# Performance work log

Hardware: AMD Instinct MI355X
Metric: run time of the kernel (lower is better)

Reference implementation:

```python
import jax, jax.numpy as jnp
import numpy as np

LN_EPS = 1e-3  # keras LayerNormalization default epsilon
LEAKY_SLOPE = 0.2  # tf 'leaky_relu' default alpha


def layer_norm(x, gamma, beta):
    mu = jnp.mean(x, axis=-1, keepdims=True)
    var = jnp.mean(jnp.square(x - mu), axis=-1, keepdims=True)
    return (x - mu) * jax.lax.rsqrt(var + LN_EPS) * gamma + beta


def attention_head(q_in, kv_in, Wk, Wv, Wq, causal):
    # q_in: [b, sq, d], kv_in: [b, sk, d]
    K = jnp.einsum('bsd,de->bse', kv_in, Wk)
    V = jnp.einsum('bsd,de->bse', kv_in, Wv)
    Q = jnp.einsum('bsd,de->bse', q_in, Wq)
    sk = K.shape[1]
    # NOTE: original scales by sqrt(window_size_keys), i.e. key seq length
    scores = jnp.einsum('bqe,bke->bqk', Q, K) / jnp.sqrt(jnp.float32(sk))
    if causal:
        sq = Q.shape[1]
        mask = jnp.triu(jnp.full((sq, sk), -jnp.inf, dtype=scores.dtype), k=1)
        scores = scores + mask
    probs = jax.nn.softmax(scores, axis=-1)
    return jnp.einsum('bqk,bke->bqe', probs, V)


def setup_inputs() -> dict:
    key = jax.random.key(0)
    ks = jax.random.split(key, 12)
    B, S, D, H = 4, 4096, 256, 400
    p = lambda k, shp: jax.random.normal(k, shp, dtype=jnp.float32) * 0.1
    return {
        'inputs': jax.random.normal(ks[0], (B, S, D), dtype=jnp.float32),
        'context_sequence': jax.random.normal(ks[1], (B, S, D), dtype=jnp.float32),
        'sa_Wk': p(ks[2], (D, D)),
        'sa_Wv': p(ks[3], (D, D)),
        'sa_Wq': p(ks[4], (D, D)),
        'ca_Wk': p(ks[5], (D, D)),
        'ca_Wv': p(ks[6], (D, D)),
        'ca_Wq': p(ks[7], (D, D)),
        'W1': p(ks[8], (D, H)),
        'b1': jnp.zeros((H,), dtype=jnp.float32),
        'W2': p(ks[9], (H, D)),
        'b2': jnp.zeros((D,), dtype=jnp.float32),
        'gamma': jnp.ones((D,), dtype=jnp.float32),
        'beta': jnp.zeros((D,), dtype=jnp.float32),
    }


def reference(inputs, context_sequence, sa_Wk, sa_Wv, sa_Wq, ca_Wk, ca_Wv, ca_Wq,
              W1, b1, W2, b2, gamma, beta):
    # 1) masked self-attention + residual + LN (shared LN params)
    in_attn = attention_head(inputs, inputs, sa_Wk, sa_Wv, sa_Wq, causal=True)
    x = layer_norm(in_attn + inputs, gamma, beta)
    # 2) unmasked cross-attention (queries = x, keys/values = context) + residual + LN
    ctx_attn = attention_head(x, context_sequence, ca_Wk, ca_Wv, ca_Wq, causal=False)
    y = layer_norm(ctx_attn + x, gamma, beta)
    # 3) FFN (Dense 400 leaky_relu -> Dense emb) + residual + LN
    h = jax.nn.leaky_relu(jnp.einsum('bsd,dh->bsh', y, W1) + b1, negative_slope=LEAKY_SLOPE)
    ff = jnp.einsum('bsh,hd->bsd', h, W2) + b2
    return layer_norm(ff + y, gamma, beta)
```

## Files before the change

kernel.cpp:

```cpp
#include <hip/hip_runtime.h>

typedef __bf16  bf16x4 __attribute__((ext_vector_type(4)));
typedef __bf16  bf16x8 __attribute__((ext_vector_type(8)));
typedef float   f32x4  __attribute__((ext_vector_type(4)));
typedef unsigned int u32;

constexpr int BM = 128, BN = 128, BK = 32;

__device__ __forceinline__ void async_cp16(const __bf16* g, __bf16* lds) {
    __builtin_amdgcn_global_load_lds(
        (const __attribute__((address_space(1))) u32*)g,
        (__attribute__((address_space(3))) u32*)lds, 16, 0, 0);
}

__device__ __forceinline__ int swz(int row, int q) {
    return row * BK + (((q + (row >> 1)) & 3) << 3);
}

template<int EPI>
__launch_bounds__(256)
__global__ void gemm_nt(const __bf16* __restrict__ Aall, const __bf16* __restrict__ Ball,
                        const float* __restrict__ bias,
                        void* __restrict__ C0, void* __restrict__ C1, void* __restrict__ C2,
                        int N, int K, long ldb, long sA, long sB, long sC,
                        int nTx, int klen, long pstrideB)
{
    const int bx = blockIdx.x;
    const int chunk = bx / nTx;
    const int n0 = (bx - chunk * nTx) * BN;
    const int m0 = blockIdx.y * BM;
    const int bz = blockIdx.z;
    const int kbase = chunk * klen;

    const __bf16* A  = Aall + (long)bz * sA;
    const __bf16* Bt = Ball + (long)bz * sB;

    __shared__ alignas(16) __bf16 As[BM * BK];
    __shared__ alignas(16) __bf16 Bs[BN * BK];

    const int tid = threadIdx.x;
    const int wave = tid >> 6, lane = tid & 63;
    const int wm = (wave >> 1) * 64, wn = (wave & 1) * 64;
    const int quad = lane >> 4, l16 = lane & 15;

    const int row0 = tid >> 2, sl0 = tid & 3;
    const int ks0 = (sl0 - (row0 >> 1)) & 3;
    const int row1 = row0 + 64;
    const int ks1 = (sl0 - (row1 >> 1)) & 3;
    const __bf16* gA0 = A  + (long)(m0 + row0) * K + kbase + ks0 * 8;
    const __bf16* gA1 = A  + (long)(m0 + row1) * K + kbase + ks1 * 8;
    const __bf16* gB0 = Bt + (long)(n0 + row0) * ldb + kbase + ks0 * 8;
    const __bf16* gB1 = Bt + (long)(n0 + row1) * ldb + kbase + ks1 * 8;
    __bf16* ldsA0 = As + wave * 512;
    __bf16* ldsA1 = As + 2048 + wave * 512;
    __bf16* ldsB0 = Bs + wave * 512;
    __bf16* ldsB1 = Bs + 2048 + wave * 512;

    f32x4 acc[4][4];
    #pragma unroll
    for (int i = 0; i < 4; i++)
        #pragma unroll
        for (int j = 0; j < 4; j++) { f32x4 z = {0.f, 0.f, 0.f, 0.f}; acc[i][j] = z; }

    for (int kk = 0; kk < klen; kk += BK) {
        __syncthreads();
        async_cp16(gA0, ldsA0);
        async_cp16(gA1, ldsA1);
        async_cp16(gB0, ldsB0);
        async_cp16(gB1, ldsB1);
        gA0 += BK; gA1 += BK; gB0 += BK; gB1 += BK;
        __syncthreads();

        bf16x8 af[4], bg[4];
        #pragma unroll
        for (int i = 0; i < 4; i++) {
            af[i] = *(const bf16x8*)(As + swz(wm + i * 16 + l16, quad));
            bg[i] = *(const bf16x8*)(Bs + swz(wn + i * 16 + l16, quad));
        }
        #pragma unroll
        for (int i = 0; i < 4; i++)
            #pragma unroll
            for (int j = 0; j < 4; j++)
                acc[i][j] = __builtin_amdgcn_mfma_f32_16x16x32_bf16(af[i], bg[j], acc[i][j], 0, 0, 0);
    }

    char* cb = (char*)C0 + (EPI == 3 ? (long)chunk * pstrideB : 0);
    #pragma unroll
    for (int j = 0; j < 4; j++) {
        const int col = n0 + wn + j * 16 + l16;
        const float bv = (EPI == 2) ? bias[col] : 0.f;
        #pragma unroll
        for (int i = 0; i < 4; i++) {
            #pragma unroll
            for (int r = 0; r < 4; r++) {
                const int row = m0 + wm + i * 16 + quad * 4 + r;
                float c = acc[i][j][r];
                if (EPI == 2) { c += bv; c = c > 0.f ? c : 0.2f * c; }
                if (EPI == 1 || EPI == 3)
                    ((__bf16*)cb)[(long)bz * sC + (long)row * N + col] = (__bf16)c;
                else if (EPI == 2)
                    ((__bf16*)cb)[(long)row * N + col] = (__bf16)c;
                else {
                    const int seg = col >> 8;
                    __bf16* dst = seg == 0 ? (__bf16*)C0 : (seg == 1 ? (__bf16*)C1 : (__bf16*)C2);
                    dst[(long)row * 256 + (col & 255)] = (__bf16)c;
                }
            }
        }
    }
}

template<int CAUSAL>
__launch_bounds__(512, 2)
__global__ void fattn(const __bf16* __restrict__ Qall, const __bf16* __restrict__ Kall,
                      const __bf16* __restrict__ Vt,
                      __bf16* __restrict__ pbuf, float* __restrict__ side,
                      int NS, long pstrideE, float scale)
{
    constexpr int S = 4096, D = 256, R = 16384;
    const int mt = CAUSAL ? (int)(gridDim.x - 1 - blockIdx.x) : (int)blockIdx.x;
    const int chunk = blockIdx.y;
    const int bz = blockIdx.z;
    const int m0 = mt * 128;

    const int T = CAUSAL ? ((m0 + 128) >> 6) : (S >> 6);
    const int t0 = chunk * T / NS;
    const int t1 = (chunk + 1) * T / NS;
    const int kbase = t0 << 6;
    const int ntile = t1 - t0;

    const __bf16* Q  = Qall + ((long)bz * S + m0) * D;
    const __bf16* Kp = Kall + (long)bz * S * D;
    const long vcol0 = (long)bz * S;

    __shared__ alignas(16) __bf16 Ks[2][16384];
    __shared__ alignas(16) __bf16 Vs[2][16384];
    __shared__ alignas(16) __bf16 Ps[128 * 64];
    __shared__ float sred[8][32];

    const int tid = threadIdx.x;
    const int wave = tid >> 6, lane = tid & 63;
    const int quad = lane >> 4, l16 = lane & 15;
    const int wq32 = (wave >> 1) * 32;
    const int wk = (wave & 1) * 32;
    const int we = (wave & 1) * 128;

    bf16x8 qf[2][8];
    #pragma unroll
    for (int i = 0; i < 2; i++)
        #pragma unroll
        for (int kd = 0; kd < 8; kd++)
            qf[i][kd] = *(const bf16x8*)(Q + (long)(wq32 + i * 16 + l16) * D + kd * 32 + quad * 8);

    const int srowK = (tid >> 2) & 63;
    const int srowV = tid >> 2;
    const int ks8 = (((tid & 3) - (tid >> 3)) & 3) << 3;
    const int wbase = (tid & ~63) * 8;

    f32x4 acc[2][8];
    #pragma unroll
    for (int i = 0; i < 2; i++)
        #pragma unroll
        for (int j = 0; j < 8; j++) { f32x4 z = {0.f, 0.f, 0.f, 0.f}; acc[i][j] = z; }
    float se[2][4] = {{0.f,0.f,0.f,0.f},{0.f,0.f,0.f,0.f}};

    auto stage = [&](int buf, int kb) {
        const __bf16* gK = Kp + (long)(kb + srowK) * D + ks8 + ((tid >> 8) << 5);
        #pragma unroll
        for (int c = 0; c < 4; c++)
            async_cp16(gK + c * 64, Ks[buf] + c * 4096 + wbase);
        const __bf16* gV = Vt + vcol0 + kb + ks8;
        #pragma unroll
        for (int c = 0; c < 4; c++)
            async_cp16(gV + (long)(((c & 1) << 7) + srowV) * R + ((c >> 1) << 5),
                       Vs[buf] + c * 4096 + wbase);
    };

    if (ntile > 0) stage(0, kbase);

    for (int t = 0; t < ntile; ++t) {
        __syncthreads();
        const int kb = kbase + (t << 6);
        if (t + 1 < ntile) stage((t + 1) & 1, kb + 64);

        const __bf16* Kb_ = Ks[t & 1];
        const __bf16* Vb_ = Vs[t & 1];

        f32x4 sacc[2][2];
        #pragma unroll
        for (int i = 0; i < 2; i++)
            #pragma unroll
            for (int j = 0; j < 2; j++) { f32x4 z = {0.f, 0.f, 0.f, 0.f}; sacc[i][j] = z; }
        #pragma unroll
        for (int kd = 0; kd < 8; kd++) {
            bf16x8 b0 = *(const bf16x8*)(Kb_ + kd * 2048 + swz(wk + l16, quad));
            bf16x8 b1 = *(const bf16x8*)(Kb_ + kd * 2048 + swz(wk + 16 + l16, quad));
            sacc[0][0] = __builtin_amdgcn_mfma_f32_16x16x32_bf16(qf[0][kd], b0, sacc[0][0], 0, 0, 0);
            sacc[1][0] = __builtin_amdgcn_mfma_f32_16x16x32_bf16(qf[1][kd], b0, sacc[1][0], 0, 0, 0);
            sacc[0][1] = __builtin_amdgcn_mfma_f32_16x16x32_bf16(qf[0][kd], b1, sacc[0][1], 0, 0, 0);
            sacc[1][1] = __builtin_amdgcn_mfma_f32_16x16x32_bf16(qf[1][kd], b1, sacc[1][1], 0, 0, 0);
        }

        const bool diag = CAUSAL && (kb >= m0);
        #pragma unroll
        for (int i = 0; i < 2; i++)
            #pragma unroll
            for (int j = 0; j < 2; j++) {
                const int kloc = wk + j * 16 + l16;
                #pragma unroll
                for (int r = 0; r < 4; r++) {
                    const int qloc = wq32 + i * 16 + quad * 4 + r;
                    float e = __expf(sacc[i][j][r] * scale);
                    if (diag && kb + kloc > m0 + qloc) e = 0.f;
                    se[i][r] += e;
                    Ps[qloc * 64 + (((kloc >> 3) ^ (qloc & 7)) << 3) + (kloc & 7)] = (__bf16)e;
                }
            }
        __syncthreads();

        #pragma unroll
        for (int kc = 0; kc < 2; kc++) {
            const int sx = (kc * 4 + quad) ^ (l16 & 7);
            bf16x8 pa0 = *(const bf16x8*)(Ps + (wq32 + l16) * 64 + (sx << 3));
            bf16x8 pa1 = *(const bf16x8*)(Ps + (wq32 + 16 + l16) * 64 + (sx << 3));
            #pragma unroll
            for (int jn = 0; jn < 8; jn++) {
                bf16x8 vb = *(const bf16x8*)(Vb_ + kc * 8192 + swz(we + jn * 16 + l16, quad));
                acc[0][jn] = __builtin_amdgcn_mfma_f32_16x16x32_bf16(pa0, vb, acc[0][jn], 0, 0, 0);
                acc[1][jn] = __builtin_amdgcn_mfma_f32_16x16x32_bf16(pa1, vb, acc[1][jn], 0, 0, 0);
            }
        }
    }

    #pragma unroll
    for (int st = 1; st < 16; st <<= 1)
        #pragma unroll
        for (int i = 0; i < 2; i++)
            #pragma unroll
            for (int r = 0; r < 4; r++) se[i][r] += __shfl_xor(se[i][r], st);
    if (l16 == 0)
        #pragma unroll
        for (int i = 0; i < 2; i++)
            #pragma unroll
            for (int r = 0; r < 4; r++)
                sred[wave][i * 16 + quad * 4 + r] = se[i][r];
    __syncthreads();
    if ((wave & 1) == 0 && l16 == 0) {
        float* sd = side + ((long)bz * 64 + chunk) * 4096 + m0 + wq32;
        #pragma unroll
        for (int i = 0; i < 2; i++)
            #pragma unroll
            for (int r = 0; r < 4; r++) {
                const int idx = i * 16 + quad * 4 + r;
                sd[idx] = sred[wave][idx] + sred[wave + 1][idx];
            }
    }

    __bf16* cb = pbuf + (long)chunk * pstrideE + ((long)bz * S + m0) * D;
    #pragma unroll
    for (int jn = 0; jn < 8; jn++) {
        const int col = we + jn * 16 + l16;
        #pragma unroll
        for (int i = 0; i < 2; i++)
            #pragma unroll
            for (int r = 0; r < 4; r++)
                cb[(long)(wq32 + i * 16 + quad * 4 + r) * D + col] = (__bf16)acc[i][jn][r];
    }
}

__global__ void reduce_inv_n(const float* __restrict__ side, float* __restrict__ inv, int lim)
{
    const int i = blockIdx.x * 256 + threadIdx.x;
    const int b = i >> 12, r = i & 4095;
    const float* sp = side + (long)b * 64 * 4096 + r;
    float s = 0.f;
    for (int t = 0; t < lim; t++) s += sp[(long)t * 4096];
    inv[i] = 1.f / s;
}

template<int NP>
__launch_bounds__(256)
__global__ void ln_res(const __bf16* __restrict__ p, long pstr,
                       const float* __restrict__ resid, const float* __restrict__ invs,
                       const float* __restrict__ bias,
                       const float* __restrict__ gamma, const float* __restrict__ beta,
                       float* __restrict__ outf, __bf16* __restrict__ outb)
{
    const int row  = blockIdx.x * 4 + (threadIdx.x >> 6);
    const int lane = threadIdx.x & 63;
    const long vi = (long)row * 64 + lane;
    float p0 = 0.f, p1 = 0.f, p2 = 0.f, p3 = 0.f;
    #pragma unroll
    for (int i = 0; i < NP; i++) {
        bf16x4 vp = ((const bf16x4*)(p + (long)i * pstr))[vi];
        p0 += (float)vp[0]; p1 += (float)vp[1]; p2 += (float)vp[2]; p3 += (float)vp[3];
    }
    if (invs) { const float iv = invs[row]; p0 *= iv; p1 *= iv; p2 *= iv; p3 *= iv; }
    float4 vr = ((const float4*)resid)[vi];
    float x0 = vr.x + p0, x1 = vr.y + p1, x2 = vr.z + p2, x3 = vr.w + p3;
    if (bias) {
        float4 vb = ((const float4*)bias)[lane];
        x0 += vb.x; x1 += vb.y; x2 += vb.z; x3 += vb.w;
    }
    float s = x0 + x1 + x2 + x3;
    #pragma unroll
    for (int off = 32; off; off >>= 1) s += __shfl_xor(s, off);
    const float mu = s * (1.f / 256.f);
    float d0 = x0 - mu, d1 = x1 - mu, d2 = x2 - mu, d3 = x3 - mu;
    float s2 = d0 * d0 + d1 * d1 + d2 * d2 + d3 * d3;
    #pragma unroll
    for (int off = 32; off; off >>= 1) s2 += __shfl_xor(s2, off);
    const float rs = rsqrtf(s2 * (1.f / 256.f) + 1e-3f);
    const float4 g  = ((const float4*)gamma)[lane];
    const float4 be = ((const float4*)beta)[lane];
    float o0 = d0 * rs * g.x + be.x, o1 = d1 * rs * g.y + be.y;
    float o2 = d2 * rs * g.z + be.z, o3 = d3 * rs * g.w + be.w;
    float4 o; o.x = o0; o.y = o1; o.z = o2; o.w = o3;
    ((float4*)outf)[vi] = o;
    if (outb) {
        bf16x4 ob; ob[0] = (__bf16)o0; ob[1] = (__bf16)o1; ob[2] = (__bf16)o2; ob[3] = (__bf16)o3;
        ((bf16x4*)outb)[vi] = ob;
    }
}

__device__ __forceinline__ void tp(const float* __restrict__ src, __bf16* __restrict__ dst,
                                   int rows, int cols, int rowsP, int i)
{
    const int c = i / rowsP, r = i - c * rowsP;
    const float v = (r < rows && c < cols) ? src[r * cols + c] : 0.f;
    dst[i] = (__bf16)v;
}

__global__ void prep_all(const float4* __restrict__ inA, const float4* __restrict__ inC,
                         bf16x4* __restrict__ outA, bf16x4* __restrict__ outC,
                         const float* __restrict__ sWq, const float* __restrict__ sWk,
                         const float* __restrict__ sWv,
                         const float* __restrict__ cWq, const float* __restrict__ cWk,
                         const float* __restrict__ cWv,
                         const float* __restrict__ W1, const float* __restrict__ W2,
                         __bf16* __restrict__ wqk_s, __bf16* __restrict__ wv_s,
                         __bf16* __restrict__ wq_c, __bf16* __restrict__ wk_c,
                         __bf16* __restrict__ wv_c,
                         __bf16* __restrict__ W1t, __bf16* __restrict__ W2t,
                         const float* __restrict__ b1, float* __restrict__ b1p)
{
    const int bx = blockIdx.x, tid = threadIdx.x;
    if (bx < 8192) {
        const bool a = bx < 4096;
        const long j = (long)(a ? bx : bx - 4096) * 256 + tid;
        float4 v = (a ? inA : inC)[j];
        bf16x4 o; o[0] = (__bf16)v.x; o[1] = (__bf16)v.y; o[2] = (__bf16)v.z; o[3] = (__bf16)v.w;
        (a ? outA : outC)[j] = o;
    }
    else if (bx < 8448)  tp(sWq, wqk_s,          256, 256, 256, (bx - 8192)  * 256 + tid);
    else if (bx < 8704)  tp(sWk, wqk_s + 65536,  256, 256, 256, (bx - 8448)  * 256 + tid);
    else if (bx < 8960)  tp(sWv, wv_s,           256, 256, 256, (bx - 8704)  * 256 + tid);
    else if (bx < 9216)  tp(cWq, wq_c,           256, 256, 256, (bx - 8960)  * 256 + tid);
    else if (bx < 9472)  tp(cWk, wk_c,           256, 256, 256, (bx - 9216)  * 256 + tid);
    else if (bx < 9728)  tp(cWv, wv_c,           256, 256, 256, (bx - 9472)  * 256 + tid);
    else if (bx < 10240) tp(W1,  W1t,            256, 400, 256, (bx - 9728)  * 256 + tid);
    else if (bx < 10752) tp(W2,  W2t,            400, 256, 512, (bx - 10240) * 256 + tid);
    else { const int i = (bx - 10752) * 256 + tid; if (i < 512) b1p[i] = (i < 400) ? b1[i] : 0.f; }
}

extern "C" void kernel_launch(void* const* d_in, const int* in_sizes, int n_in,
                              void* d_out, int out_size, void* d_ws, size_t ws_size,
                              hipStream_t stream)
{
    constexpr int B = 4, S = 4096, D = 256, H = 400, Hp = 512;
    constexpr int R = B * S;
    constexpr float SCALE = 1.f / 64.f;
    constexpr int NSc = 4;
    constexpr int NSx = 2;
    constexpr int NSf = 2;

    const float* inputs = (const float*)d_in[0];
    const float* ctx    = (const float*)d_in[1];
    const float* sa_Wk  = (const float*)d_in[2];
    const float* sa_Wv  = (const float*)d_in[3];
    const float* sa_Wq  = (const float*)d_in[4];
    const float* ca_Wk  = (const float*)d_in[5];
    const float* ca_Wv  = (const float*)d_in[6];
    const float* ca_Wq  = (const float*)d_in[7];
    const float* W1     = (const float*)d_in[8];
    const float* b1     = (const float*)d_in[9];
    const float* W2     = (const float*)d_in[10];
    const float* b2     = (const float*)d_in[11];
    const float* gamma  = (const float*)d_in[12];
    const float* beta   = (const float*)d_in[13];
    float* out = (float*)d_out;

    char* ws = (char*)d_ws;
    size_t off = 0;
    auto alloc = [&](size_t bytes) -> char* {
        char* p = ws + off; off += (bytes + 255) & ~size_t(255); return p;
    };
    __bf16* bfA  = (__bf16*)alloc((size_t)R * D * 2);
    __bf16* bfC  = (__bf16*)alloc((size_t)R * D * 2);
    __bf16* Qb   = (__bf16*)alloc((size_t)R * D * 2);
    __bf16* Kb   = (__bf16*)alloc((size_t)R * D * 2);
    __bf16* Vt   = (__bf16*)alloc((size_t)D * R * 2);
    __bf16* h    = (__bf16*)alloc((size_t)R * Hp * 2);
    float*  x    = (float*)alloc((size_t)R * D * 4);
    float*  y    = (float*)alloc((size_t)R * D * 4);
    float*  side = (float*)alloc((size_t)B * 64 * S * 4);
    float*  invb = (float*)alloc((size_t)B * S * 4);
    __bf16* wqk_s = (__bf16*)alloc((size_t)2 * D * D * 2);
    __bf16* wv_s  = (__bf16*)alloc((size_t)D * D * 2);
    __bf16* wq_c  = (__bf16*)alloc((size_t)D * D * 2);
    __bf16* wk_c  = (__bf16*)alloc((size_t)D * D * 2);
    __bf16* wv_c  = (__bf16*)alloc((size_t)D * D * 2);
    __bf16* W1t  = (__bf16*)alloc((size_t)Hp * D * 2);
    __bf16* W2t  = (__bf16*)alloc((size_t)D * Hp * 2);
    float*  b1p  = (float*)alloc((size_t)Hp * 4);

    const size_t PBb = (size_t)R * D * 2;
    __bf16* pbuf = (__bf16*)alloc((size_t)4 * PBb);
    if (off > ws_size) return;
    const long PBe = (long)R * D;

    __bf16* xbf = bfA;
    __bf16* ybf = bfC;

    const dim3 blk(256);
    const dim3 blk512(512);

    auto launch_ln = [&](int np, const float* res, const float* invs, const float* bias,
                         float* of, __bf16* ob) {
        if (np == 4)      ln_res<4><<<R / 4, blk, 0, stream>>>(pbuf, PBe, res, invs, bias, gamma, beta, of, ob);
        else if (np == 2) ln_res<2><<<R / 4, blk, 0, stream>>>(pbuf, PBe, res, invs, bias, gamma, beta, of, ob);
        else              ln_res<1><<<R / 4, blk, 0, stream>>>(pbuf, PBe, res, invs, bias, gamma, beta, of, ob);
    };

    prep_all<<<10754, blk, 0, stream>>>((const float4*)inputs, (const float4*)ctx,
        (bf16x4*)bfA, (bf16x4*)bfC, sa_Wq, sa_Wk, sa_Wv, ca_Wq, ca_Wk, ca_Wv, W1, W2,
        wqk_s, wv_s, wq_c, wk_c, wv_c, W1t, W2t, b1, b1p);

    gemm_nt<4><<<dim3(4, 128, 1), blk, 0, stream>>>(bfA, wqk_s, nullptr,
        Qb, Kb, nullptr, 2 * D, D, D, 0, 0, 0, 4, D, 0);
    gemm_nt<1><<<dim3(128, 2, 1), blk, 0, stream>>>(wv_s, bfA, nullptr,
        Vt, nullptr, nullptr, R, D, D, 0, 0, 0, 128, D, 0);
    fattn<1><<<dim3(32, NSc, B), blk512, 0, stream>>>(Qb, Kb, Vt, pbuf, side, NSc, PBe, SCALE);
    reduce_inv_n<<<R / 256, blk, 0, stream>>>(side, invb, NSc);
    launch_ln(NSc, inputs, invb, nullptr, x, xbf);

    gemm_nt<1><<<dim3(2, 128, 1), blk, 0, stream>>>(xbf, wq_c, nullptr,
        Qb, nullptr, nullptr, D, D, D, 0, 0, 0, 2, D, 0);
    gemm_nt<1><<<dim3(2, 128, 1), blk, 0, stream>>>(bfC, wk_c, nullptr,
        Kb, nullptr, nullptr, D, D, D, 0, 0, 0, 2, D, 0);
    gemm_nt<1><<<dim3(128, 2, 1), blk, 0, stream>>>(wv_c, bfC, nullptr,
        Vt, nullptr, nullptr, R, D, D, 0, 0, 0, 128, D, 0);
    fattn<0><<<dim3(32, NSx, B), blk512, 0, stream>>>(Qb, Kb, Vt, pbuf, side, NSx, PBe, SCALE);
    reduce_inv_n<<<R / 256, blk, 0, stream>>>(side, invb, NSx);
    launch_ln(NSx, x, invb, nullptr, y, ybf);

    gemm_nt<2><<<dim3(4, 128, 1), blk, 0, stream>>>(ybf, W1t, b1p,
        h, nullptr, nullptr, Hp, D, D, 0, 0, 0, 4, D, 0);
    gemm_nt<3><<<dim3(2 * NSf, 128, 1), blk, 0, stream>>>(h, W2t, nullptr,
        pbuf, nullptr, nullptr, D, Hp, Hp, 0, 0, 0, 2, Hp / NSf, (long)PBb);
    launch_ln(NSf, y, nullptr, b2, out, nullptr);
}
```

Before: 409.6 us.

## Prefetch two K/V tiles ahead with fine-grained waitcnt barriers in attention loop

Restructures the attention K/V loop so two tiles are in flight. After each tile is consumed, the next-next tile is staged into the freed buffer, and the loop waits only on vmcnt for the older tile instead of a full __syncthreads. It also raises wave priority around the MFMA sections with s_setprio. This aims to hide global-to-LDS latency better, at the cost of extra barriers per iteration and reliance on manual vmcnt counts matching the number of outstanding loads.

```diff
diff --git a/kernel.cpp b/kernel.cpp
--- a/kernel.cpp
+++ b/kernel.cpp
@@ -16,6 +16,11 @@
 __device__ __forceinline__ int swz(int row, int q) {
     return row * BK + (((q + (row >> 1)) & 3) << 3);
 }
+
+#define ASM_LGKM0 asm volatile("s_waitcnt lgkmcnt(0)" ::: "memory")
+#define ASM_VM8   asm volatile("s_waitcnt vmcnt(8)" ::: "memory")
+#define ASM_VM0   asm volatile("s_waitcnt vmcnt(0)" ::: "memory")
+#define SBAR()    do { __builtin_amdgcn_s_barrier(); asm volatile("" ::: "memory"); } while (0)
 
 template<int EPI>
 __launch_bounds__(256)
@@ -176,21 +181,25 @@
                        Vs[buf] + c * 4096 + wbase);
     };
 
-    if (ntile > 0) stage(0, kbase);
+    if (ntile > 0) {
+        stage(0, kbase);
+        if (ntile > 1) { stage(1, kbase + 64); ASM_VM8; }
+        else           { ASM_VM0; }
+        SBAR();
+    }
 
     for (int t = 0; t < ntile; ++t) {
-        __syncthreads();
+        const int cur = t & 1;
         const int kb = kbase + (t << 6);
-        if (t + 1 < ntile) stage((t + 1) & 1, kb + 64);
-
-        const __bf16* Kb_ = Ks[t & 1];
-        const __bf16* Vb_ = Vs[t & 1];
+        const __bf16* Kb_ = Ks[cur];
+        const __bf16* Vb_ = Vs[cur];
 
         f32x4 sacc[2][2];
         #pragma unroll
         for (int i = 0; i < 2; i++)
             #pragma unroll
             for (int j = 0; j < 2; j++) { f32x4 z = {0.f, 0.f, 0.f, 0.f}; sacc[i][j] = z; }
+        __builtin_amdgcn_s_setprio(1);
         #pragma unroll
         for (int kd = 0; kd < 8; kd++) {
             bf16x8 b0 = *(const bf16x8*)(Kb_ + kd * 2048 + swz(wk + l16, quad));
@@ -200,6 +209,7 @@
             sacc[0][1] = __builtin_amdgcn_mfma_f32_16x16x32_bf16(qf[0][kd], b1, sacc[0][1], 0, 0, 0);
             sacc[1][1] = __builtin_amdgcn_mfma_f32_16x16x32_bf16(qf[1][kd], b1, sacc[1][1], 0, 0, 0);
         }
+        __builtin_amdgcn_s_setprio(0);
 
         const bool diag = CAUSAL && (kb >= m0);
         #pragma unroll
@@ -216,8 +226,9 @@
                     Ps[qloc * 64 + (((kloc >> 3) ^ (qloc & 7)) << 3) + (kloc & 7)] = (__bf16)e;
                 }
             }
-        __syncthreads();
-
+        ASM_LGKM0; SBAR();
+
+        __builtin_amdgcn_s_setprio(1);
         #pragma unroll
         for (int kc = 0; kc < 2; kc++) {
             const int sx = (kc * 4 + quad) ^ (l16 & 7);
@@ -229,6 +240,14 @@
                 acc[0][jn] = __builtin_amdgcn_mfma_f32_16x16x32_bf16(pa0, vb, acc[0][jn], 0, 0, 0);
                 acc[1][jn] = __builtin_amdgcn_mfma_f32_16x16x32_bf16(pa1, vb, acc[1][jn], 0, 0, 0);
             }
+        }
+        __builtin_amdgcn_s_setprio(0);
+        ASM_LGKM0; SBAR();
+
+        if (t + 1 < ntile) {
+            if (t + 2 < ntile) { stage(cur, kbase + ((t + 2) << 6)); ASM_VM8; }
+            else               { ASM_VM0; }
+            SBAR();
         }
     }
 
```

Result: no change. 406.8 us (-0.7%).

## Halve attention key tile to 32 to raise occupancy and split cross-attn further

Applied to the files above, without the earlier changes.

Shrinks the flash-attention key/value tile from 64 to 32 keys. This halves the K/V/P shared-memory buffers and the score accumulators, and the launch bounds now request 4 blocks per CU instead of 2. The P buffer swizzle and the staging index math are reworked for the narrower tile. The cross-attention key split count also goes from 2 to 4. In exchange there are twice as many tile iterations, each with two barriers and less MFMA work to hide latency, and more partial results to combine.

```diff
diff --git a/kernel.cpp b/kernel.cpp
--- a/kernel.cpp
+++ b/kernel.cpp
@@ -111,7 +111,7 @@
 }
 
 template<int CAUSAL>
-__launch_bounds__(512, 2)
+__launch_bounds__(512, 4)
 __global__ void fattn(const __bf16* __restrict__ Qall, const __bf16* __restrict__ Kall,
                       const __bf16* __restrict__ Vt,
                       __bf16* __restrict__ pbuf, float* __restrict__ side,
@@ -123,26 +123,26 @@
     const int bz = blockIdx.z;
     const int m0 = mt * 128;
 
-    const int T = CAUSAL ? ((m0 + 128) >> 6) : (S >> 6);
+    const int T = CAUSAL ? ((m0 + 128) >> 5) : (S >> 5);
     const int t0 = chunk * T / NS;
     const int t1 = (chunk + 1) * T / NS;
-    const int kbase = t0 << 6;
+    const int kbase = t0 << 5;
     const int ntile = t1 - t0;
 
     const __bf16* Q  = Qall + ((long)bz * S + m0) * D;
     const __bf16* Kp = Kall + (long)bz * S * D;
     const long vcol0 = (long)bz * S;
 
-    __shared__ alignas(16) __bf16 Ks[2][16384];
-    __shared__ alignas(16) __bf16 Vs[2][16384];
-    __shared__ alignas(16) __bf16 Ps[128 * 64];
+    __shared__ alignas(16) __bf16 Ks[2][8192];
+    __shared__ alignas(16) __bf16 Vs[2][8192];
+    __shared__ alignas(16) __bf16 Ps[128 * 32];
     __shared__ float sred[8][32];
 
     const int tid = threadIdx.x;
     const int wave = tid >> 6, lane = tid & 63;
     const int quad = lane >> 4, l16 = lane & 15;
     const int wq32 = (wave >> 1) * 32;
-    const int wk = (wave & 1) * 32;
+    const int wk16 = (wave & 1) * 16;
     const int we = (wave & 1) * 128;
 
     bf16x8 qf[2][8];
@@ -152,7 +152,7 @@
         for (int kd = 0; kd < 8; kd++)
             qf[i][kd] = *(const bf16x8*)(Q + (long)(wq32 + i * 16 + l16) * D + kd * 32 + quad * 8);
 
-    const int srowK = (tid >> 2) & 63;
+    const int srowK = (tid >> 2) & 31;
     const int srowV = tid >> 2;
     const int ks8 = (((tid & 3) - (tid >> 3)) & 3) << 3;
     const int wbase = (tid & ~63) * 8;
@@ -165,67 +165,57 @@
     float se[2][4] = {{0.f,0.f,0.f,0.f},{0.f,0.f,0.f,0.f}};
 
     auto stage = [&](int buf, int kb) {
-        const __bf16* gK = Kp + (long)(kb + srowK) * D + ks8 + ((tid >> 8) << 5);
-        #pragma unroll
-        for (int c = 0; c < 4; c++)
-            async_cp16(gK + c * 64, Ks[buf] + c * 4096 + wbase);
-        const __bf16* gV = Vt + vcol0 + kb + ks8;
-        #pragma unroll
-        for (int c = 0; c < 4; c++)
-            async_cp16(gV + (long)(((c & 1) << 7) + srowV) * R + ((c >> 1) << 5),
-                       Vs[buf] + c * 4096 + wbase);
+        const __bf16* gK = Kp + (long)(kb + srowK) * D + ks8 + ((tid >> 7) << 5);
+        async_cp16(gK,       Ks[buf] + wbase);
+        async_cp16(gK + 128, Ks[buf] + 4096 + wbase);
+        const __bf16* gV = Vt + vcol0 + kb + ks8 + (long)srowV * R;
+        async_cp16(gV,                 Vs[buf] + wbase);
+        async_cp16(gV + (long)128 * R, Vs[buf] + 4096 + wbase);
     };
 
     if (ntile > 0) stage(0, kbase);
 
     for (int t = 0; t < ntile; ++t) {
+        const int cur = t & 1;
+        const int kb = kbase + (t << 5);
         __syncthreads();
-        const int kb = kbase + (t << 6);
-        if (t + 1 < ntile) stage((t + 1) & 1, kb + 64);
-
-        const __bf16* Kb_ = Ks[t & 1];
-        const __bf16* Vb_ = Vs[t & 1];
-
-        f32x4 sacc[2][2];
-        #pragma unroll
-        for (int i = 0; i < 2; i++)
-            #pragma unroll
-            for (int j = 0; j < 2; j++) { f32x4 z = {0.f, 0.f, 0.f, 0.f}; sacc[i][j] = z; }
+        if (t + 1 < ntile) stage(cur ^ 1, kb + 32);
+
+        const __bf16* Kb_ = Ks[cur];
+        const __bf16* Vb_ = Vs[cur];
+
+        f32x4 sacc[2];
+        #pragma unroll
+        for (int i = 0; i < 2; i++) { f32x4 z = {0.f, 0.f, 0.f, 0.f}; sacc[i] = z; }
         #pragma unroll
         for (int kd = 0; kd < 8; kd++) {
-            bf16x8 b0 = *(const bf16x8*)(Kb_ + kd * 2048 + swz(wk + l16, quad));
-            bf16x8 b1 = *(const bf16x8*)(Kb_ + kd * 2048 + swz(wk + 16 + l16, quad));
-            sacc[0][0] = __builtin_amdgcn_mfma_f32_16x16x32_bf16(qf[0][kd], b0, sacc[0][0], 0, 0, 0);
-            sacc[1][0] = __builtin_amdgcn_mfma_f32_16x16x32_bf16(qf[1][kd], b0, sacc[1][0], 0, 0, 0);
-            sacc[0][1] = __builtin_amdgcn_mfma_f32_16x16x32_bf16(qf[0][kd], b1, sacc[0][1], 0, 0, 0);
-            sacc[1][1] = __builtin_amdgcn_mfma_f32_16x16x32_bf16(qf[1][kd], b1, sacc[1][1], 0, 0, 0);
+            bf16x8 b0 = *(const bf16x8*)(Kb_ + kd * 1024 + swz(wk16 + l16, quad));
+            sacc[0] = __builtin_amdgcn_mfma_f32_16x16x32_bf16(qf[0][kd], b0, sacc[0], 0, 0, 0);
+            sacc[1] = __builtin_amdgcn_mfma_f32_16x16x32_bf16(qf[1][kd], b0, sacc[1], 0, 0, 0);
         }
 
         const bool diag = CAUSAL && (kb >= m0);
-        #pragma unroll
-        for (int i = 0; i < 2; i++)
-            #pragma unroll
-            for (int j = 0; j < 2; j++) {
-                const int kloc = wk + j * 16 + l16;
-                #pragma unroll
-                for (int r = 0; r < 4; r++) {
-                    const int qloc = wq32 + i * 16 + quad * 4 + r;
-                    float e = __expf(sacc[i][j][r] * scale);
-                    if (diag && kb + kloc > m0 + qloc) e = 0.f;
-                    se[i][r] += e;
-                    Ps[qloc * 64 + (((kloc >> 3) ^ (qloc & 7)) << 3) + (kloc & 7)] = (__bf16)e;
-                }
+        const int kloc = wk16 + l16;
+        #pragma unroll
+        for (int i = 0; i < 2; i++) {
+            #pragma unroll
+            for (int r = 0; r < 4; r++) {
+                const int qloc = wq32 + i * 16 + quad * 4 + r;
+                float e = __expf(sacc[i][r] * scale);
+                if (diag && kb + kloc > m0 + qloc) e = 0.f;
+                se[i][r] += e;
+                Ps[qloc * 32 + (((kloc >> 3) ^ ((qloc >> 1) & 3)) << 3) + (kloc & 7)] = (__bf16)e;
             }
+        }
         __syncthreads();
 
-        #pragma unroll
-        for (int kc = 0; kc < 2; kc++) {
-            const int sx = (kc * 4 + quad) ^ (l16 & 7);
-            bf16x8 pa0 = *(const bf16x8*)(Ps + (wq32 + l16) * 64 + (sx << 3));
-            bf16x8 pa1 = *(const bf16x8*)(Ps + (wq32 + 16 + l16) * 64 + (sx << 3));
+        {
+            const int q0 = wq32 + l16, q1 = wq32 + 16 + l16;
+            bf16x8 pa0 = *(const bf16x8*)(Ps + q0 * 32 + ((quad ^ ((q0 >> 1) & 3)) << 3));
+            bf16x8 pa1 = *(const bf16x8*)(Ps + q1 * 32 + ((quad ^ ((q1 >> 1) & 3)) << 3));
             #pragma unroll
             for (int jn = 0; jn < 8; jn++) {
-                bf16x8 vb = *(const bf16x8*)(Vb_ + kc * 8192 + swz(we + jn * 16 + l16, quad));
+                bf16x8 vb = *(const bf16x8*)(Vb_ + swz(we + jn * 16 + l16, quad));
                 acc[0][jn] = __builtin_amdgcn_mfma_f32_16x16x32_bf16(pa0, vb, acc[0][jn], 0, 0, 0);
                 acc[1][jn] = __builtin_amdgcn_mfma_f32_16x16x32_bf16(pa1, vb, acc[1][jn], 0, 0, 0);
             }
@@ -371,7 +361,7 @@
     constexpr int R = B * S;
     constexpr float SCALE = 1.f / 64.f;
     constexpr int NSc = 4;
-    constexpr int NSx = 2;
+    constexpr int NSx = 4;
     constexpr int NSf = 2;
 
     const float* inputs = (const float*)d_in[0];
```

After: 726.5 us. 77.4% more time.
